# Kernel optimization log

Hardware: AMD Instinct MI355X
Metric: run time of the kernel (lower is better)

Reference implementation:

```python
import jax, jax.numpy as jnp
import numpy as np

B = 16384
OBS = 568        # 36 self features + 19 * 28 other-agent features
H = 256          # hidden_dim
SELF_DIM = 36
OTHER_DIM = 28
N_OTHER = (OBS - SELF_DIM) // OTHER_DIM  # 19


def _linear_init(key, fan_in, fan_out):
    # torch nn.Linear default: U(-1/sqrt(fan_in), 1/sqrt(fan_in))
    kw, kb = jax.random.split(key)
    s = 1.0 / np.sqrt(fan_in)
    W = jax.random.uniform(kw, (fan_in, fan_out), jnp.float32, -s, s)
    b = jax.random.uniform(kb, (fan_out,), jnp.float32, -s, s)
    return W, b


def setup_inputs() -> dict:
    key = jax.random.key(0)
    ks = jax.random.split(key, 10)
    x = jax.random.normal(ks[0], (B, OBS), jnp.float32)
    eps = jax.random.normal(ks[1], (B, H), jnp.float32)
    W_mu, b_mu = _linear_init(ks[2], OBS, H)
    W_var, b_var = _linear_init(ks[3], OBS, H)
    W_self, b_self = _linear_init(ks[4], SELF_DIM, H)
    W_other, b_other = _linear_init(ks[5], OTHER_DIM, H)
    W_q, b_q = _linear_init(ks[6], H, H)
    W_k, b_k = _linear_init(ks[7], H, H)
    W_v, b_v = _linear_init(ks[8], 2 * H, H)
    W_a, b_a = _linear_init(ks[9], 2 * H, H)
    return {"x": x, "eps": eps,
            "W_mu": W_mu, "b_mu": b_mu, "W_var": W_var, "b_var": b_var,
            "W_self": W_self, "b_self": b_self, "W_other": W_other, "b_other": b_other,
            "W_q": W_q, "b_q": b_q, "W_k": W_k, "b_k": b_k,
            "W_v": W_v, "b_v": b_v, "W_a": W_a, "b_a": b_a}


def reference(x, eps, W_mu, b_mu, W_var, b_var, W_self, b_self,
              W_other, b_other, W_q, b_q, W_k, b_k, W_v, b_v, W_a, b_a):
    relu = jax.nn.relu
    # VAE reparameterization (detach=False path)
    mu = x @ W_mu + b_mu                                  # [B, H]
    log_var = x @ W_var + b_var                           # [B, H]
    z = eps * jnp.exp(0.5 * log_var) + mu                 # [B, H]

    self_info = x[:, :SELF_DIM]                           # [B, 36]
    agents_info = x[:, SELF_DIM:].reshape(B, N_OTHER, OTHER_DIM)  # [B, N, 28]

    self_em = relu(self_info @ W_self + b_self)           # [B, H]
    other_ems = relu(agents_info @ W_other + b_other)     # [B, N, H]

    q = relu(z @ W_q + b_q)                               # [B, H]
    k = relu(other_ems @ W_k + b_k)                       # [B, N, H]
    v_in = jnp.concatenate(
        [other_ems, jnp.broadcast_to(self_em[:, None, :], (B, N_OTHER, H))], axis=-1)
    v = relu(v_in @ W_v + b_v)                            # [B, N, H]

    scores = jnp.einsum('bh,bnh->bn', q, k) / np.sqrt(H)  # [B, N]
    att_weight = jax.nn.softmax(scores, axis=-1)          # [B, N]
    h = jnp.einsum('bn,bnh->bh', att_weight, v)           # [B, H]

    out = relu(jnp.concatenate([h, self_em], axis=-1) @ W_a + b_a)  # [B, H]
    return out, att_weight[:, None, :]                    # att: [B, 1, N]
```

## Files before the change

kernel.cpp:

```cpp
#include <hip/hip_runtime.h>

typedef __bf16 bf16;
typedef __bf16 bf16x4 __attribute__((ext_vector_type(4)));
typedef __bf16 bf16x8 __attribute__((ext_vector_type(8)));
typedef float  f32x4  __attribute__((ext_vector_type(4)));

#define NB    16384
#define NOBS  568
#define NH    256
#define NAG   19

#define OFF_WT_MU    0u
#define OFF_WT_VAR   294912u
#define OFF_WT_SELF  589824u
#define OFF_WT_OTHER 622592u
#define OFF_WT_Q     638976u
#define OFF_WT_K     770048u
#define OFF_WT_V1    901120u
#define OFF_WT_V2    1032192u
#define OFF_WT_A1    1163264u
#define OFF_WT_A2    1294336u
#define OFF_Z        1425408u
#define OFF_SELF     9814016u
#define OFF_Q        18202624u
#define OFF_SV       26591232u
#define OFF_H        34979840u

static __device__ __forceinline__ unsigned short bfbits(float v) {
  bf16 b = (bf16)v;
  union { bf16 b; unsigned short u; } cvt; cvt.b = b; return cvt.u;
}

__global__ __launch_bounds__(256) void wprep(
    const float* __restrict__ Wmu, const float* __restrict__ Wvar,
    const float* __restrict__ Wself, const float* __restrict__ Wother,
    const float* __restrict__ Wq, const float* __restrict__ Wk,
    const float* __restrict__ Wv, const float* __restrict__ Wa, char* wsb)
{
  const float* src; bf16* dst; int K, Kp; bool chunked = false;
  switch (blockIdx.y) {
    case 0: src = Wmu;        dst = (bf16*)(wsb + OFF_WT_MU);    K = 568; Kp = 576; break;
    case 1: src = Wvar;       dst = (bf16*)(wsb + OFF_WT_VAR);   K = 568; Kp = 576; break;
    case 2: src = Wself;      dst = (bf16*)(wsb + OFF_WT_SELF);  K = 36;  Kp = 64;  break;
    case 3: src = Wother;     dst = (bf16*)(wsb + OFF_WT_OTHER); K = 28;  Kp = 32;  break;
    case 4: src = Wq;         dst = (bf16*)(wsb + OFF_WT_Q);     K = 256; Kp = 256; break;
    case 5: src = Wk;         dst = (bf16*)(wsb + OFF_WT_K);     K = 256; Kp = 256; chunked = true; break;
    case 6: src = Wv;         dst = (bf16*)(wsb + OFF_WT_V1);    K = 256; Kp = 256; chunked = true; break;
    case 7: src = Wv + 65536; dst = (bf16*)(wsb + OFF_WT_V2);    K = 256; Kp = 256; break;
    case 8: src = Wa;         dst = (bf16*)(wsb + OFF_WT_A1);    K = 256; Kp = 256; break;
    default: src = Wa + 65536; dst = (bf16*)(wsb + OFF_WT_A2);   K = 256; Kp = 256; break;
  }
  int total = 256 * Kp;
  if (chunked) {
    for (int i = blockIdx.x * 256 + threadIdx.x; i < total; i += gridDim.x * 256) {
      int ch = i >> 13, n = (i >> 5) & 255, kk = i & 31;
      int k = ch * 32 + kk;
      dst[i] = (bf16)src[k * 256 + n];
    }
  } else {
    for (int i = blockIdx.x * 256 + threadIdx.x; i < total; i += gridDim.x * 256) {
      int n = i / Kp, k = i - n * Kp;
      dst[i] = (k < K) ? (bf16)src[k * 256 + n] : (bf16)0.f;
    }
  }
}

__global__ __launch_bounds__(256, 3) void gemm_zself(
    const float* __restrict__ x,
    const bf16* __restrict__ WtMu, const bf16* __restrict__ WtVar,
    const bf16* __restrict__ WtSelf,
    const float* __restrict__ b_mu, const float* __restrict__ b_var,
    const float* __restrict__ b_self, const float* __restrict__ eps,
    bf16* __restrict__ zout, bf16* __restrict__ selfout)
{
  __shared__ bf16 ldsA[64 * 40];
  __shared__ bf16 ldsB[128 * 40];
  __shared__ bf16 ldsB2[128 * 40];

  const int tid = threadIdx.x;
  const int wave = tid >> 6;
  const int lane = tid & 63;
  const int quad = lane >> 4;
  const int m = lane & 15;
  const int rowbase = blockIdx.x * 64;
  const int colbase = (blockIdx.y & 1) * 128;
  const bool isZ = blockIdx.y < 2;
  const int K = isZ ? 576 : 64;
  const bf16* __restrict__ Wt = isZ ? WtMu : WtSelf;
  const float* __restrict__ bias = isZ ? b_mu : b_self;

  f32x4 acc[8], accB[8];
  const f32x4 z4 = {0.f, 0.f, 0.f, 0.f};
#pragma unroll
  for (int ct = 0; ct < 8; ++ct) { acc[ct] = z4; accB[ct] = z4; }

  for (int kc = 0; kc < K; kc += 32) {
    __syncthreads();
    {
#pragma unroll
      for (int it = 0; it < 2; ++it) {
        int p = tid + 256 * it;
        int r = p >> 3, fs = p & 7;
        int k = kc + fs * 4;
        const float* src = x + (size_t)(rowbase + r) * 568 + k;
        float v0, v1, v2, v3;
        if (k + 4 <= 568) {
          float4 v = *(const float4*)src;
          v0 = v.x; v1 = v.y; v2 = v.z; v3 = v.w;
        } else {
          v0 = (k + 0 < 568) ? src[0] : 0.f;
          v1 = (k + 1 < 568) ? src[1] : 0.f;
          v2 = (k + 2 < 568) ? src[2] : 0.f;
          v3 = (k + 3 < 568) ? src[3] : 0.f;
        }
        bf16x4 o = {(bf16)v0, (bf16)v1, (bf16)v2, (bf16)v3};
        *(bf16x4*)(ldsA + r * 40 + fs * 4) = o;
      }
    }
#pragma unroll
    for (int it = 0; it < 2; ++it) {
      int p = tid + 256 * it;
      int n = p >> 2, f = p & 3;
      *(bf16x8*)(ldsB + n * 40 + f * 8) =
          *(const bf16x8*)(Wt + (size_t)(colbase + n) * K + kc + f * 8);
    }
    if (isZ) {
#pragma unroll
      for (int it = 0; it < 2; ++it) {
        int p = tid + 256 * it;
        int n = p >> 2, f = p & 3;
        *(bf16x8*)(ldsB2 + n * 40 + f * 8) =
            *(const bf16x8*)(WtVar + (size_t)(colbase + n) * 576 + kc + f * 8);
      }
    }
    __syncthreads();
    bf16x8 afrag = *(const bf16x8*)(ldsA + (wave * 16 + m) * 40 + quad * 8);
#pragma unroll
    for (int ct = 0; ct < 8; ++ct) {
      bf16x8 bfrag = *(const bf16x8*)(ldsB + (ct * 16 + m) * 40 + quad * 8);
      acc[ct] = __builtin_amdgcn_mfma_f32_16x16x32_bf16(afrag, bfrag, acc[ct], 0, 0, 0);
      if (isZ) {
        bf16x8 b2 = *(const bf16x8*)(ldsB2 + (ct * 16 + m) * 40 + quad * 8);
        accB[ct] = __builtin_amdgcn_mfma_f32_16x16x32_bf16(afrag, b2, accB[ct], 0, 0, 0);
      }
    }
  }
#pragma unroll
  for (int ct = 0; ct < 8; ++ct) {
    const int col = colbase + ct * 16 + m;
    const float bv = bias[col];
#pragma unroll
    for (int r = 0; r < 4; ++r) {
      const size_t row = (size_t)rowbase + wave * 16 + quad * 4 + r;
      float v = acc[ct][r] + bv;
      if (isZ) {
        float lv = accB[ct][r] + b_var[col];
        float zz = eps[row * 256 + col] * __expf(0.5f * lv) + v;
        zout[row * 256 + col] = (bf16)zz;
      } else {
        selfout[row * 256 + col] = (bf16)(v > 0.f ? v : 0.f);
      }
    }
  }
}

__global__ __launch_bounds__(256, 4) void gemm_qsv(
    const bf16* __restrict__ zb, const bf16* __restrict__ selfb,
    const bf16* __restrict__ WtQ, const bf16* __restrict__ WtV2,
    const float* __restrict__ b_q, const float* __restrict__ b_v,
    bf16* __restrict__ qout, bf16* __restrict__ svout)
{
  __shared__ bf16 ldsA[64 * 40];
  __shared__ bf16 ldsB[128 * 40];

  const int tid = threadIdx.x;
  const int wave = tid >> 6;
  const int lane = tid & 63;
  const int quad = lane >> 4;
  const int m = lane & 15;
  const int rowbase = blockIdx.x * 64;
  const int colbase = (blockIdx.y & 1) * 128;
  const bool isQ = blockIdx.y < 2;
  const bf16* __restrict__ Ap = isQ ? zb : selfb;
  const bf16* __restrict__ Wt = isQ ? WtQ : WtV2;
  const float* __restrict__ bias = isQ ? b_q : b_v;
  bf16* __restrict__ outp = isQ ? qout : svout;

  f32x4 acc[8];
  const f32x4 z4 = {0.f, 0.f, 0.f, 0.f};
#pragma unroll
  for (int ct = 0; ct < 8; ++ct) acc[ct] = z4;

  for (int kc = 0; kc < 256; kc += 32) {
    __syncthreads();
    {
      int p = tid;
      int r = p >> 2, f = p & 3;
      *(bf16x8*)(ldsA + r * 40 + f * 8) =
          *(const bf16x8*)(Ap + (size_t)(rowbase + r) * 256 + kc + f * 8);
    }
#pragma unroll
    for (int it = 0; it < 2; ++it) {
      int p = tid + 256 * it;
      int n = p >> 2, f = p & 3;
      *(bf16x8*)(ldsB + n * 40 + f * 8) =
          *(const bf16x8*)(Wt + (size_t)(colbase + n) * 256 + kc + f * 8);
    }
    __syncthreads();
    bf16x8 afrag = *(const bf16x8*)(ldsA + (wave * 16 + m) * 40 + quad * 8);
#pragma unroll
    for (int ct = 0; ct < 8; ++ct) {
      bf16x8 bfrag = *(const bf16x8*)(ldsB + (ct * 16 + m) * 40 + quad * 8);
      acc[ct] = __builtin_amdgcn_mfma_f32_16x16x32_bf16(afrag, bfrag, acc[ct], 0, 0, 0);
    }
  }
#pragma unroll
  for (int ct = 0; ct < 8; ++ct) {
    const int col = colbase + ct * 16 + m;
    const float bv = bias[col];
#pragma unroll
    for (int r = 0; r < 4; ++r) {
      const size_t row = (size_t)rowbase + wave * 16 + quad * 4 + r;
      float v = acc[ct][r] + bv;
      if (isQ) v = (v > 0.f ? v : 0.f);
      outp[row * 256 + col] = (bf16)v;
    }
  }
}

template<bool UNUSED>
__global__ __launch_bounds__(256, 2) void gemm_dualA(
    const bf16* __restrict__ A1, const bf16* __restrict__ A2,
    const bf16* __restrict__ Wt1, const bf16* __restrict__ Wt2,
    const float* __restrict__ bias, float* __restrict__ outp)
{
  __shared__ bf16 ldsA[64 * 40];
  __shared__ bf16 ldsB[128 * 40];

  const int tid = threadIdx.x;
  const int wave = tid >> 6;
  const int lane = tid & 63;
  const int quad = lane >> 4;
  const int m = lane & 15;
  const int rowbase = blockIdx.x * 64;
  const int colbase = blockIdx.y * 128;

  f32x4 acc[8];
  const f32x4 z4 = {0.f, 0.f, 0.f, 0.f};
#pragma unroll
  for (int ct = 0; ct < 8; ++ct) acc[ct] = z4;

  for (int pass = 0; pass < 2; ++pass) {
    const bf16* Ap = (pass == 0) ? A1 : A2;
    const bf16* Wp = (pass == 0) ? Wt1 : Wt2;
    for (int kc = 0; kc < 256; kc += 32) {
      __syncthreads();
      {
        int p = tid;
        int r = p >> 2, f = p & 3;
        *(bf16x8*)(ldsA + r * 40 + f * 8) =
            *(const bf16x8*)(Ap + (size_t)(rowbase + r) * 256 + kc + f * 8);
      }
#pragma unroll
      for (int it = 0; it < 2; ++it) {
        int p = tid + 256 * it;
        int n = p >> 2, f = p & 3;
        *(bf16x8*)(ldsB + n * 40 + f * 8) =
            *(const bf16x8*)(Wp + (size_t)(colbase + n) * 256 + kc + f * 8);
      }
      __syncthreads();
      bf16x8 afrag = *(const bf16x8*)(ldsA + (wave * 16 + m) * 40 + quad * 8);
#pragma unroll
      for (int ct = 0; ct < 8; ++ct) {
        bf16x8 bfrag = *(const bf16x8*)(ldsB + (ct * 16 + m) * 40 + quad * 8);
        acc[ct] = __builtin_amdgcn_mfma_f32_16x16x32_bf16(afrag, bfrag, acc[ct], 0, 0, 0);
      }
    }
  }
#pragma unroll
  for (int ct = 0; ct < 8; ++ct) {
    const int col = colbase + ct * 16 + m;
    const float bv = bias[col];
#pragma unroll
    for (int r = 0; r < 4; ++r) {
      const size_t row = (size_t)rowbase + wave * 16 + quad * 4 + r;
      float v = acc[ct][r] + bv;
      outp[row * 256 + col] = (v > 0.f ? v : 0.f);
    }
  }
}

__global__ __launch_bounds__(256, 3) void k_fused(
    const float* __restrict__ x, const bf16* __restrict__ qb,
    const bf16* __restrict__ svb,
    const bf16* __restrict__ WtOther, const float* __restrict__ b_other,
    const bf16* __restrict__ WtKc, const float* __restrict__ b_k,
    const bf16* __restrict__ WtVc,
    float* __restrict__ att_out, bf16* __restrict__ hb)
{
  __shared__ bf16 ldsO[80 * 264];
  __shared__ bf16 ldsA1[80 * 40];
  __shared__ bf16 qh16[1024];
  __shared__ bf16 svl16[1024];
  float* spart = (float*)ldsA1;
  float* attl  = (float*)ldsA1 + 320;

  const int tid = threadIdx.x, wave = tid >> 6, lane = tid & 63;
  const int quad = lane >> 4, m = lane & 15;
  const int b0 = blockIdx.x * 4;

  for (int i = tid; i < 512; i += 256) {
    ((unsigned*)qh16)[i]  = ((const unsigned*)(qb  + (size_t)b0 * 256))[i];
    ((unsigned*)svl16)[i] = ((const unsigned*)(svb + (size_t)b0 * 256))[i];
  }
  for (int i = tid; i < 80 * 16; i += 256) {
    int r = i >> 4, kk = (i & 15) * 2;
    int n = r >> 2, bb = r & 3;
    float v0 = 0.f, v1 = 0.f;
    if (n < 19) {
      const float* base = x + (size_t)(b0 + bb) * NOBS + 36 + n * 28;
      if (kk < 28) v0 = base[kk];
      if (kk + 1 < 28) v1 = base[kk + 1];
    }
    unsigned u0 = bfbits(v0), u1 = bfbits(v1);
    *(unsigned*)(ldsA1 + r * 40 + kk) = u0 | (u1 << 16);
  }
  __syncthreads();

  const f32x4 z4 = {0.f, 0.f, 0.f, 0.f};

  {
    float bo[4];
#pragma unroll
    for (int c = 0; c < 4; ++c) bo[c] = b_other[(4 * wave + c) * 16 + m];
    f32x4 acc1[5][4];
    bf16x8 bfr[4];
#pragma unroll
    for (int c = 0; c < 4; ++c)
      bfr[c] = *(const bf16x8*)(WtOther + ((4 * wave + c) * 16 + m) * 32 + quad * 8);
#pragma unroll
    for (int rt = 0; rt < 5; ++rt) {
      bf16x8 a = *(const bf16x8*)(ldsA1 + (rt * 16 + m) * 40 + quad * 8);
#pragma unroll
      for (int c = 0; c < 4; ++c)
        acc1[rt][c] = __builtin_amdgcn_mfma_f32_16x16x32_bf16(a, bfr[c], z4, 0, 0, 0);
    }
#pragma unroll
    for (int rt = 0; rt < 5; ++rt)
#pragma unroll
      for (int c = 0; c < 4; ++c) {
        int col = (4 * wave + c) * 16 + m;
#pragma unroll
        for (int r = 0; r < 4; ++r) {
          float v = acc1[rt][c][r] + bo[c];
          v = v > 0.f ? v : 0.f;
          unsigned u = bfbits(v);
          unsigned other = (unsigned)__shfl_xor((int)u, 1, 64);
          if ((m & 1) == 0) {
            int rowl = rt * 16 + quad * 4 + r;
            *(unsigned*)(ldsO + rowl * 264 + col) = u | (other << 16);
          }
        }
      }
  }
  __syncthreads();

  float qreg[4][4];
#pragma unroll
  for (int c = 0; c < 4; ++c) {
    int col = (4 * wave + c) * 16 + m;
#pragma unroll
    for (int r = 0; r < 4; ++r) qreg[c][r] = (float)qh16[r * 256 + col];
  }
  float bkreg[4];
#pragma unroll
  for (int c = 0; c < 4; ++c) bkreg[c] = b_k[(4 * wave + c) * 16 + m];

  {
    f32x4 aK[5][4];
#pragma unroll
    for (int rt = 0; rt < 5; ++rt)
#pragma unroll
      for (int c = 0; c < 4; ++c) aK[rt][c] = z4;

    bf16x8 bK[4];
#pragma unroll
    for (int c = 0; c < 4; ++c)
      bK[c] = *(const bf16x8*)(WtKc + ((4 * wave + c) * 16 + m) * 32 + quad * 8);
#pragma unroll 1
    for (int ch = 0; ch < 8; ++ch) {
      bf16x8 bN[4];
      if (ch < 7) {
#pragma unroll
        for (int c = 0; c < 4; ++c)
          bN[c] = *(const bf16x8*)(WtKc + (size_t)(ch + 1) * 8192 + ((4 * wave + c) * 16 + m) * 32 + quad * 8);
      }
      const int kc = ch * 32;
#pragma unroll
      for (int rt = 0; rt < 5; ++rt) {
        bf16x8 a = *(const bf16x8*)(ldsO + (rt * 16 + m) * 264 + kc + quad * 8);
#pragma unroll
        for (int c = 0; c < 4; ++c)
          aK[rt][c] = __builtin_amdgcn_mfma_f32_16x16x32_bf16(a, bK[c], aK[rt][c], 0, 0, 0);
      }
      if (ch < 7) {
#pragma unroll
        for (int c = 0; c < 4; ++c) bK[c] = bN[c];
      }
    }

#pragma unroll
    for (int rt = 0; rt < 5; ++rt) {
      float part[4] = {0.f, 0.f, 0.f, 0.f};
#pragma unroll
      for (int c = 0; c < 4; ++c) {
#pragma unroll
        for (int r = 0; r < 4; ++r) {
          float kv = aK[rt][c][r] + bkreg[c];
          kv = kv > 0.f ? kv : 0.f;
          part[r] += kv * qreg[c][r];
        }
      }
#pragma unroll
      for (int r = 0; r < 4; ++r) {
        float p = part[r];
        p += __shfl_xor(p, 1, 64);
        p += __shfl_xor(p, 2, 64);
        p += __shfl_xor(p, 4, 64);
        p += __shfl_xor(p, 8, 64);
        if (m == 0) spart[wave * 80 + rt * 16 + quad * 4 + r] = p;
      }
    }
  }
  __syncthreads();
  if (tid < 4) {
    float sc[19];
    float mx = -1e30f;
#pragma unroll
    for (int j = 0; j < 19; ++j) {
      int row = j * 4 + tid;
      float s = (spart[row] + spart[80 + row] + spart[160 + row] + spart[240 + row]) * 0.0625f;
      sc[j] = s; mx = fmaxf(mx, s);
    }
    float sum = 0.f;
#pragma unroll
    for (int j = 0; j < 19; ++j) { float e = __expf(sc[j] - mx); sc[j] = e; sum += e; }
    float inv = 1.f / sum;
#pragma unroll
    for (int j = 0; j < 19; ++j) {
      float a = sc[j] * inv;
      attl[j * 4 + tid] = a;
      att_out[(size_t)(b0 + tid) * 19 + j] = a;
    }
    attl[76 + tid] = 0.f;
  }
  __syncthreads();

  float svreg[4][4];
#pragma unroll
  for (int c = 0; c < 4; ++c) {
    int col = (4 * wave + c) * 16 + m;
#pragma unroll
    for (int r = 0; r < 4; ++r) svreg[c][r] = (float)svl16[r * 256 + col];
  }

  {
    f32x4 aV[5][4];
#pragma unroll
    for (int rt = 0; rt < 5; ++rt)
#pragma unroll
      for (int c = 0; c < 4; ++c) aV[rt][c] = z4;

    bf16x8 bV[4];
#pragma unroll
    for (int c = 0; c < 4; ++c)
      bV[c] = *(const bf16x8*)(WtVc + ((4 * wave + c) * 16 + m) * 32 + quad * 8);
#pragma unroll 1
    for (int ch = 0; ch < 8; ++ch) {
      bf16x8 bN[4];
      if (ch < 7) {
#pragma unroll
        for (int c = 0; c < 4; ++c)
          bN[c] = *(const bf16x8*)(WtVc + (size_t)(ch + 1) * 8192 + ((4 * wave + c) * 16 + m) * 32 + quad * 8);
      }
      const int kc = ch * 32;
#pragma unroll
      for (int rt = 0; rt < 5; ++rt) {
        bf16x8 a = *(const bf16x8*)(ldsO + (rt * 16 + m) * 264 + kc + quad * 8);
#pragma unroll
        for (int c = 0; c < 4; ++c)
          aV[rt][c] = __builtin_amdgcn_mfma_f32_16x16x32_bf16(a, bV[c], aV[rt][c], 0, 0, 0);
      }
      if (ch < 7) {
#pragma unroll
        for (int c = 0; c < 4; ++c) bV[c] = bN[c];
      }
    }

    float hacc[4][4];
#pragma unroll
    for (int c = 0; c < 4; ++c)
#pragma unroll
      for (int r = 0; r < 4; ++r) hacc[c][r] = 0.f;
#pragma unroll
    for (int rt = 0; rt < 5; ++rt) {
      float av[4];
#pragma unroll
      for (int r = 0; r < 4; ++r) av[r] = attl[rt * 16 + quad * 4 + r];
#pragma unroll
      for (int c = 0; c < 4; ++c) {
#pragma unroll
        for (int r = 0; r < 4; ++r) {
          float v = aV[rt][c][r] + svreg[c][r];
          v = v > 0.f ? v : 0.f;
          hacc[c][r] += v * av[r];
        }
      }
    }
#pragma unroll
    for (int c = 0; c < 4; ++c)
#pragma unroll
      for (int r = 0; r < 4; ++r) {
        float h = hacc[c][r];
        h += __shfl_xor(h, 16, 64);
        h += __shfl_xor(h, 32, 64);
        if (quad == 0) qh16[r * 256 + (4 * wave + c) * 16 + m] = (bf16)h;
      }
  }
  __syncthreads();
  for (int i = tid; i < 512; i += 256)
    ((unsigned*)(hb + (size_t)b0 * 256))[i] = ((const unsigned*)qh16)[i];
}

extern "C" void kernel_launch(void* const* d_in, const int* in_sizes, int n_in,
                              void* d_out, int out_size, void* d_ws, size_t ws_size,
                              hipStream_t stream) {
  (void)in_sizes; (void)n_in; (void)out_size; (void)ws_size;
  const float* x      = (const float*)d_in[0];
  const float* eps    = (const float*)d_in[1];
  const float* W_mu   = (const float*)d_in[2];
  const float* b_mu   = (const float*)d_in[3];
  const float* W_var  = (const float*)d_in[4];
  const float* b_var  = (const float*)d_in[5];
  const float* W_self = (const float*)d_in[6];
  const float* b_self = (const float*)d_in[7];
  const float* W_other= (const float*)d_in[8];
  const float* b_other= (const float*)d_in[9];
  const float* W_q    = (const float*)d_in[10];
  const float* b_q    = (const float*)d_in[11];
  const float* W_k    = (const float*)d_in[12];
  const float* b_k    = (const float*)d_in[13];
  const float* W_v    = (const float*)d_in[14];
  const float* b_v    = (const float*)d_in[15];
  const float* W_a    = (const float*)d_in[16];
  const float* b_a    = (const float*)d_in[17];

  char* wsb = (char*)d_ws;
  bf16* WtMu    = (bf16*)(wsb + OFF_WT_MU);
  bf16* WtVar   = (bf16*)(wsb + OFF_WT_VAR);
  bf16* WtSelf  = (bf16*)(wsb + OFF_WT_SELF);
  bf16* WtOther = (bf16*)(wsb + OFF_WT_OTHER);
  bf16* WtQ     = (bf16*)(wsb + OFF_WT_Q);
  bf16* WtK     = (bf16*)(wsb + OFF_WT_K);
  bf16* WtV1    = (bf16*)(wsb + OFF_WT_V1);
  bf16* WtV2    = (bf16*)(wsb + OFF_WT_V2);
  bf16* WtA1    = (bf16*)(wsb + OFF_WT_A1);
  bf16* WtA2    = (bf16*)(wsb + OFF_WT_A2);
  bf16* zbuf    = (bf16*)(wsb + OFF_Z);
  bf16* selfbuf = (bf16*)(wsb + OFF_SELF);
  bf16* qbuf    = (bf16*)(wsb + OFF_Q);
  bf16* svbuf   = (bf16*)(wsb + OFF_SV);
  bf16* hbuf    = (bf16*)(wsb + OFF_H);

  float* out = (float*)d_out;
  float* att_out = out + (size_t)NB * 256;

  dim3 blk(256);
  wprep<<<dim3(160, 10), blk, 0, stream>>>(W_mu, W_var, W_self, W_other, W_q, W_k, W_v, W_a, wsb);
  gemm_zself<<<dim3(NB / 64, 4), blk, 0, stream>>>(x, WtMu, WtVar, WtSelf,
                                                   b_mu, b_var, b_self, eps, zbuf, selfbuf);
  gemm_qsv<<<dim3(NB / 64, 4), blk, 0, stream>>>(zbuf, selfbuf, WtQ, WtV2,
                                                 b_q, b_v, qbuf, svbuf);
  k_fused<<<NB / 4, blk, 0, stream>>>(x, qbuf, svbuf, WtOther, b_other, WtK, b_k,
                                      WtV1, att_out, hbuf);
  gemm_dualA<true><<<dim3(NB / 64, 2), blk, 0, stream>>>(hbuf, selfbuf, WtA1, WtA2, b_a, out);
}
```

Baseline: 338.1 us.

## Split fused attention block into concurrent K and V wave groups with 512 threads

The fused attention kernel grows from 256 to 512 threads. Waves 0-3 compute the K projection and the scores while waves 4-7 compute the V projection at the same time, instead of one set of waves doing K and then V in sequence. The aim is to overlap the two MFMA GEMMs and shorten the serial chain in each block. The software prefetch of weight chunks is dropped, and the higher launch bounds may limit registers per thread and cause spills.

```diff
diff --git a/kernel.cpp b/kernel.cpp
--- a/kernel.cpp
+++ b/kernel.cpp
@@ -290,7 +290,7 @@
   }
 }
 
-__global__ __launch_bounds__(256, 3) void k_fused(
+__global__ __launch_bounds__(512, 4) void k_fused(
     const float* __restrict__ x, const bf16* __restrict__ qb,
     const bf16* __restrict__ svb,
     const bf16* __restrict__ WtOther, const float* __restrict__ b_other,
@@ -308,12 +308,12 @@
   const int tid = threadIdx.x, wave = tid >> 6, lane = tid & 63;
   const int quad = lane >> 4, m = lane & 15;
   const int b0 = blockIdx.x * 4;
-
-  for (int i = tid; i < 512; i += 256) {
-    ((unsigned*)qh16)[i]  = ((const unsigned*)(qb  + (size_t)b0 * 256))[i];
-    ((unsigned*)svl16)[i] = ((const unsigned*)(svb + (size_t)b0 * 256))[i];
-  }
-  for (int i = tid; i < 80 * 16; i += 256) {
+  const int kvw = wave & 3;
+  const bool isV = wave >= 4;
+
+  ((unsigned*)qh16)[tid]  = ((const unsigned*)(qb  + (size_t)b0 * 256))[tid];
+  ((unsigned*)svl16)[tid] = ((const unsigned*)(svb + (size_t)b0 * 256))[tid];
+  for (int i = tid; i < 80 * 16; i += 512) {
     int r = i >> 4, kk = (i & 15) * 2;
     int n = r >> 2, bb = r & 3;
     float v0 = 0.f, v1 = 0.f;
@@ -330,26 +330,27 @@
   const f32x4 z4 = {0.f, 0.f, 0.f, 0.f};
 
   {
-    float bo[4];
-#pragma unroll
-    for (int c = 0; c < 4; ++c) bo[c] = b_other[(4 * wave + c) * 16 + m];
-    f32x4 acc1[5][4];
-    bf16x8 bfr[4];
-#pragma unroll
-    for (int c = 0; c < 4; ++c)
-      bfr[c] = *(const bf16x8*)(WtOther + ((4 * wave + c) * 16 + m) * 32 + quad * 8);
+    float bo[2];
+    bf16x8 bfr[2];
+#pragma unroll
+    for (int c = 0; c < 2; ++c) {
+      int col = (2 * wave + c) * 16 + m;
+      bo[c] = b_other[col];
+      bfr[c] = *(const bf16x8*)(WtOther + col * 32 + quad * 8);
+    }
+    f32x4 acc1[5][2];
 #pragma unroll
     for (int rt = 0; rt < 5; ++rt) {
       bf16x8 a = *(const bf16x8*)(ldsA1 + (rt * 16 + m) * 40 + quad * 8);
 #pragma unroll
-      for (int c = 0; c < 4; ++c)
+      for (int c = 0; c < 2; ++c)
         acc1[rt][c] = __builtin_amdgcn_mfma_f32_16x16x32_bf16(a, bfr[c], z4, 0, 0, 0);
     }
 #pragma unroll
     for (int rt = 0; rt < 5; ++rt)
 #pragma unroll
-      for (int c = 0; c < 4; ++c) {
-        int col = (4 * wave + c) * 16 + m;
+      for (int c = 0; c < 2; ++c) {
+        int col = (2 * wave + c) * 16 + m;
 #pragma unroll
         for (int r = 0; r < 4; ++r) {
           float v = acc1[rt][c][r] + bo[c];
@@ -365,50 +366,41 @@
   }
   __syncthreads();
 
-  float qreg[4][4];
-#pragma unroll
-  for (int c = 0; c < 4; ++c) {
-    int col = (4 * wave + c) * 16 + m;
-#pragma unroll
-    for (int r = 0; r < 4; ++r) qreg[c][r] = (float)qh16[r * 256 + col];
-  }
-  float bkreg[4];
-#pragma unroll
-  for (int c = 0; c < 4; ++c) bkreg[c] = b_k[(4 * wave + c) * 16 + m];
+  f32x4 acc[5][4];
+#pragma unroll
+  for (int rt = 0; rt < 5; ++rt)
+#pragma unroll
+    for (int c = 0; c < 4; ++c) acc[rt][c] = z4;
 
   {
-    f32x4 aK[5][4];
-#pragma unroll
-    for (int rt = 0; rt < 5; ++rt)
-#pragma unroll
-      for (int c = 0; c < 4; ++c) aK[rt][c] = z4;
-
-    bf16x8 bK[4];
-#pragma unroll
-    for (int c = 0; c < 4; ++c)
-      bK[c] = *(const bf16x8*)(WtKc + ((4 * wave + c) * 16 + m) * 32 + quad * 8);
+    const bf16* __restrict__ Bc = isV ? WtVc : WtKc;
+    const int cb = (kvw * 64 + m) * 32;
 #pragma unroll 1
     for (int ch = 0; ch < 8; ++ch) {
-      bf16x8 bN[4];
-      if (ch < 7) {
-#pragma unroll
-        for (int c = 0; c < 4; ++c)
-          bN[c] = *(const bf16x8*)(WtKc + (size_t)(ch + 1) * 8192 + ((4 * wave + c) * 16 + m) * 32 + quad * 8);
-      }
+      bf16x8 bB[4];
+#pragma unroll
+      for (int c = 0; c < 4; ++c)
+        bB[c] = *(const bf16x8*)(Bc + (size_t)ch * 8192 + cb + c * 512 + quad * 8);
       const int kc = ch * 32;
 #pragma unroll
       for (int rt = 0; rt < 5; ++rt) {
         bf16x8 a = *(const bf16x8*)(ldsO + (rt * 16 + m) * 264 + kc + quad * 8);
 #pragma unroll
         for (int c = 0; c < 4; ++c)
-          aK[rt][c] = __builtin_amdgcn_mfma_f32_16x16x32_bf16(a, bK[c], aK[rt][c], 0, 0, 0);
-      }
-      if (ch < 7) {
-#pragma unroll
-        for (int c = 0; c < 4; ++c) bK[c] = bN[c];
-      }
-    }
-
+          acc[rt][c] = __builtin_amdgcn_mfma_f32_16x16x32_bf16(a, bB[c], acc[rt][c], 0, 0, 0);
+      }
+    }
+  }
+
+  if (!isV) {
+    float qreg[4][4], bkreg[4];
+#pragma unroll
+    for (int c = 0; c < 4; ++c) {
+      int col = (4 * wave + c) * 16 + m;
+      bkreg[c] = b_k[col];
+#pragma unroll
+      for (int r = 0; r < 4; ++r) qreg[c][r] = (float)qh16[r * 256 + col];
+    }
 #pragma unroll
     for (int rt = 0; rt < 5; ++rt) {
       float part[4] = {0.f, 0.f, 0.f, 0.f};
@@ -416,7 +408,7 @@
       for (int c = 0; c < 4; ++c) {
 #pragma unroll
         for (int r = 0; r < 4; ++r) {
-          float kv = aK[rt][c][r] + bkreg[c];
+          float kv = acc[rt][c][r] + bkreg[c];
           kv = kv > 0.f ? kv : 0.f;
           part[r] += kv * qreg[c][r];
         }
@@ -456,47 +448,14 @@
   }
   __syncthreads();
 
-  float svreg[4][4];
-#pragma unroll
-  for (int c = 0; c < 4; ++c) {
-    int col = (4 * wave + c) * 16 + m;
-#pragma unroll
-    for (int r = 0; r < 4; ++r) svreg[c][r] = (float)svl16[r * 256 + col];
-  }
-
-  {
-    f32x4 aV[5][4];
-#pragma unroll
-    for (int rt = 0; rt < 5; ++rt)
-#pragma unroll
-      for (int c = 0; c < 4; ++c) aV[rt][c] = z4;
-
-    bf16x8 bV[4];
-#pragma unroll
-    for (int c = 0; c < 4; ++c)
-      bV[c] = *(const bf16x8*)(WtVc + ((4 * wave + c) * 16 + m) * 32 + quad * 8);
-#pragma unroll 1
-    for (int ch = 0; ch < 8; ++ch) {
-      bf16x8 bN[4];
-      if (ch < 7) {
-#pragma unroll
-        for (int c = 0; c < 4; ++c)
-          bN[c] = *(const bf16x8*)(WtVc + (size_t)(ch + 1) * 8192 + ((4 * wave + c) * 16 + m) * 32 + quad * 8);
-      }
-      const int kc = ch * 32;
-#pragma unroll
-      for (int rt = 0; rt < 5; ++rt) {
-        bf16x8 a = *(const bf16x8*)(ldsO + (rt * 16 + m) * 264 + kc + quad * 8);
-#pragma unroll
-        for (int c = 0; c < 4; ++c)
-          aV[rt][c] = __builtin_amdgcn_mfma_f32_16x16x32_bf16(a, bV[c], aV[rt][c], 0, 0, 0);
-      }
-      if (ch < 7) {
-#pragma unroll
-        for (int c = 0; c < 4; ++c) bV[c] = bN[c];
-      }
-    }
-
+  if (isV) {
+    float svreg[4][4];
+#pragma unroll
+    for (int c = 0; c < 4; ++c) {
+      int col = (4 * kvw + c) * 16 + m;
+#pragma unroll
+      for (int r = 0; r < 4; ++r) svreg[c][r] = (float)svl16[r * 256 + col];
+    }
     float hacc[4][4];
 #pragma unroll
     for (int c = 0; c < 4; ++c)
@@ -511,7 +470,7 @@
       for (int c = 0; c < 4; ++c) {
 #pragma unroll
         for (int r = 0; r < 4; ++r) {
-          float v = aV[rt][c][r] + svreg[c][r];
+          float v = acc[rt][c][r] + svreg[c][r];
           v = v > 0.f ? v : 0.f;
           hacc[c][r] += v * av[r];
         }
@@ -524,12 +483,11 @@
         float h = hacc[c][r];
         h += __shfl_xor(h, 16, 64);
         h += __shfl_xor(h, 32, 64);
-        if (quad == 0) qh16[r * 256 + (4 * wave + c) * 16 + m] = (bf16)h;
+        if (quad == 0) qh16[r * 256 + (4 * kvw + c) * 16 + m] = (bf16)h;
       }
   }
   __syncthreads();
-  for (int i = tid; i < 512; i += 256)
-    ((unsigned*)(hb + (size_t)b0 * 256))[i] = ((const unsigned*)qh16)[i];
+  ((unsigned*)(hb + (size_t)b0 * 256))[tid] = ((const unsigned*)qh16)[tid];
 }
 
 extern "C" void kernel_launch(void* const* d_in, const int* in_sizes, int n_in,
@@ -581,7 +539,7 @@
                                                    b_mu, b_var, b_self, eps, zbuf, selfbuf);
   gemm_qsv<<<dim3(NB / 64, 4), blk, 0, stream>>>(zbuf, selfbuf, WtQ, WtV2,
                                                  b_q, b_v, qbuf, svbuf);
-  k_fused<<<NB / 4, blk, 0, stream>>>(x, qbuf, svbuf, WtOther, b_other, WtK, b_k,
-                                      WtV1, att_out, hbuf);
+  k_fused<<<NB / 4, dim3(512), 0, stream>>>(x, qbuf, svbuf, WtOther, b_other, WtK, b_k,
+                                            WtV1, att_out, hbuf);
   gemm_dualA<true><<<dim3(NB / 64, 2), blk, 0, stream>>>(hbuf, selfbuf, WtA1, WtA2, b_a, out);
 }
```

After: 342.7 us. About the same (+1.4%).
